# Performance work log

Hardware: AMD Instinct MI355X
Metric: run time of the kernel (lower is better)

Reference implementation:

```python
import jax, jax.numpy as jnp
import numpy as np

B, SQ, SK, D = 8, 2048, 768, 768  # SK must equal D for layer_combine concat to typecheck


def setup_inputs() -> dict:
    key = jax.random.key(0)
    ks = jax.random.split(key, 13)
    s = 0.02
    return {
        "query": jax.random.normal(ks[0], (B, SQ, D), jnp.float32),
        "key_matrix": jax.random.normal(ks[1], (B, SK, D), jnp.float32),
        "value_matrix": jax.random.normal(ks[2], (B, SK, D), jnp.float32),
        "prev_layer": jax.random.normal(ks[3], (SK, D), jnp.float32) * s,
        "attention_mask": jax.random.randint(ks[4], (B, 1, SK), 0, 2, jnp.int32),
        "Wq": jax.random.normal(ks[5], (D, D), jnp.float32) * s,
        "bq": jax.random.normal(ks[6], (D,), jnp.float32) * s,
        "Wk": jax.random.normal(ks[7], (D, D), jnp.float32) * s,
        "bk": jax.random.normal(ks[8], (D,), jnp.float32) * s,
        "Wv": jax.random.normal(ks[9], (D, D), jnp.float32) * s,
        "bv": jax.random.normal(ks[10], (D,), jnp.float32) * s,
        "Wc": jax.random.normal(ks[11], (D, 2 * D), jnp.float32) * s,
        "bc": jax.random.normal(ks[12], (D,), jnp.float32) * s,
    }


def reference(query, key_matrix, value_matrix, prev_layer, attention_mask,
              Wq, bq, Wk, bk, Wv, bv, Wc, bc):
    # Linear projections (torch Linear: x @ W.T + b)
    Q = query @ Wq.T + bq                      # [B, SQ, D]
    K = key_matrix @ Wk.T + bk                 # [B, SK, D]
    V = value_matrix @ Wv.T + bv               # computed but unused when prev_layer given (faithful)
    scale = 1.0 / np.sqrt(D).astype(np.float32)
    scores = jnp.einsum('bqd,bkd->bqk', Q, K) * scale  # [B, SQ, SK]
    scores = jnp.where(attention_mask == 0, jnp.float32(-1e9), scores)
    # prev-layer integration: matmul + concat + linear combine
    layer_attn = scores @ prev_layer           # [B, SQ, D]
    combined = jnp.concatenate([scores, layer_attn], axis=-1)  # [B, SQ, 2D]
    out = combined @ Wc.T + bc                 # [B, SQ, D]
    return out
```

## Files before the change

kernel.cpp:

```cpp
#include <hip/hip_runtime.h>
#include <hip/hip_bf16.h>


typedef __attribute__((ext_vector_type(8))) short short8;
typedef __attribute__((ext_vector_type(4))) float f32x4;

#define SCALE 0.03608439182435161f

__device__ inline unsigned short f2bf(float x) {
  unsigned int u = __builtin_bit_cast(unsigned int, x);
  u = (u + 0x7fffu + ((u >> 16) & 1u)) >> 16;
  return (unsigned short)u;
}
__device__ inline float bf2f(unsigned short h) {
  return __builtin_bit_cast(float, ((unsigned int)h) << 16);
}

__global__ void k_cvt(const float* __restrict__ s, unsigned short* __restrict__ d, int n4) {
  int i = blockIdx.x * 256 + threadIdx.x;
  if (i >= n4) return;
  float4 v = reinterpret_cast<const float4*>(s)[i];
  reinterpret_cast<ushort4*>(d)[i] = make_ushort4(f2bf(v.x), f2bf(v.y), f2bf(v.z), f2bf(v.w));
}

__global__ void k_prep(const float* __restrict__ Wk, const float* __restrict__ prev,
                       const float* __restrict__ Wc,
                       unsigned short* __restrict__ Wk_bf,
                       unsigned short* __restrict__ prev_bf,
                       unsigned short* __restrict__ Wc2_bf) {
  int g = blockIdx.x;
  int region = g / 576;
  int idx = (g - region * 576) * 256 + threadIdx.x;
  float4 v;
  unsigned short* dst;
  if (region == 0)      { v = reinterpret_cast<const float4*>(Wk)[idx];   dst = Wk_bf; }
  else if (region == 1) { v = reinterpret_cast<const float4*>(prev)[idx]; dst = prev_bf; }
  else {
    int r = idx / 192, c4 = (idx - r * 192) * 4;
    v = *reinterpret_cast<const float4*>(Wc + (long long)r * 1536 + 768 + c4);
    dst = Wc2_bf;
  }
  reinterpret_cast<ushort4*>(dst)[idx] = make_ushort4(f2bf(v.x), f2bf(v.y), f2bf(v.z), f2bf(v.w));
}

__global__ void k_transpose(const float* __restrict__ src, unsigned short* __restrict__ dst) {
  __shared__ float t[64][65];
  int bx = blockIdx.x * 64, by = blockIdx.y * 64;
  int tx = threadIdx.x & 63, ty = threadIdx.x >> 6;
  #pragma unroll
  for (int i = 0; i < 64; i += 4)
    t[ty + i][tx] = src[(long long)(by + ty + i) * 768 + bx + tx];
  __syncthreads();
  #pragma unroll
  for (int i = 0; i < 64; i += 4)
    dst[(long long)(bx + ty + i) * 768 + by + tx] = f2bf(t[tx][ty + i]);
}

template <int MODE, int BM, int BN>
__global__ __launch_bounds__(256) void gemm_nt(
    const unsigned short* __restrict__ A, long long aStr, int lda,
    const unsigned short* __restrict__ B, long long bStr, int ldb,
    float* __restrict__ Cf, unsigned short* __restrict__ Cbf,
    long long cStr, int ldc,
    const float* __restrict__ aux, const int* __restrict__ mask)
{
  constexpr int BK = 64;
  constexpr int MI = BM / 32;
  constexpr int NJ = BN / 32;
  constexpr int AG = BM * 8, BG = BN * 8;
  __shared__ __align__(16) char As[BM * BK * 2];
  __shared__ __align__(16) char Bs[BN * BK * 2];

  const int gx = gridDim.x, gy = gridDim.y;
  const int nwg = gx * gy * (int)gridDim.z;
  int lin = blockIdx.x + gx * (blockIdx.y + gy * blockIdx.z);
  int qq = nwg >> 3, rr = nwg & 7, xcd = lin & 7, loc = lin >> 3;
  int swz = (xcd < rr ? xcd * (qq + 1) : rr * (qq + 1) + (xcd - rr) * qq) + loc;
  int bz = swz / (gx * gy);
  int rem = swz - bz * gx * gy;
  int by = rem / gx, bx = rem - by * gx;

  const int b = bz;
  const unsigned short* Ab = A + (long long)b * aStr;
  const unsigned short* Bb = B + (long long)b * bStr;
  const int m0 = by * BM, n0 = bx * BN;

  const int tid = threadIdx.x;
  const int w = tid >> 6, lane = tid & 63;
  const int wr = w >> 1, wc = w & 1;
  const int fr = lane & 15, fq = lane >> 4;

  f32x4 acc[MI][NJ] = {};

  for (int kt = 0; kt < 768; kt += BK) {
    __syncthreads();
    #pragma unroll
    for (int t = 0; t < AG / 256; ++t) {
      int g = t * 256 + tid;
      int row = g >> 3, s = g & 7;
      int sg = (s - row) & 7;
      const unsigned short* ga = Ab + (long long)(m0 + row) * lda + kt + sg * 8;
      __builtin_amdgcn_global_load_lds(
          (const __attribute__((address_space(1))) void*)ga,
          (__attribute__((address_space(3))) void*)(As + g * 16), 16, 0, 0);
    }
    #pragma unroll
    for (int t = 0; t < BG / 256; ++t) {
      int g = t * 256 + tid;
      int row = g >> 3, s = g & 7;
      int sg = (s - row) & 7;
      const unsigned short* gb = Bb + (long long)(n0 + row) * ldb + kt + sg * 8;
      __builtin_amdgcn_global_load_lds(
          (const __attribute__((address_space(1))) void*)gb,
          (__attribute__((address_space(3))) void*)(Bs + g * 16), 16, 0, 0);
    }
    __syncthreads();

    #pragma unroll
    for (int kk = 0; kk < 2; ++kk) {
      short8 af[MI], bfr[NJ];
      #pragma unroll
      for (int i = 0; i < MI; ++i) {
        int r = wr * (BM / 2) + i * 16 + fr;
        int sgi = ((kk * 4 + fq) + r) & 7;
        af[i] = *reinterpret_cast<const short8*>(As + r * 128 + sgi * 16);
      }
      #pragma unroll
      for (int j = 0; j < NJ; ++j) {
        int r = wc * (BN / 2) + j * 16 + fr;
        int sgj = ((kk * 4 + fq) + r) & 7;
        bfr[j] = *reinterpret_cast<const short8*>(Bs + r * 128 + sgj * 16);
      }
      #pragma unroll
      for (int i = 0; i < MI; ++i)
        #pragma unroll
        for (int j = 0; j < NJ; ++j)
          acc[i][j] = __builtin_amdgcn_mfma_f32_16x16x32_bf16(af[i], bfr[j], acc[i][j], 0, 0, 0);
    }
  }

  const int* mb = (MODE == 1) ? (mask + b * 768) : nullptr;
  #pragma unroll
  for (int i = 0; i < MI; ++i)
    #pragma unroll
    for (int j = 0; j < NJ; ++j)
      #pragma unroll
      for (int r = 0; r < 4; ++r) {
        int row = m0 + wr * (BM / 2) + i * 16 + fq * 4 + r;
        int col = n0 + wc * (BN / 2) + j * 16 + fr;
        float v = acc[i][j][r];
        if constexpr (MODE == 0) {
          v += aux[(long long)row * 1536 + col];
          Cf[(long long)row * 768 + col] = v;
          Cbf[(long long)row * 768 + col] = f2bf(v);
        } else if constexpr (MODE == 1) {
          v += aux[row];
          if (mb[col] == 0) v = 0.0f;
          Cbf[(long long)b * cStr + (long long)row * ldc + col] = f2bf(v);
        } else if constexpr (MODE == 2 || MODE == 3) {
          Cbf[(long long)b * cStr + (long long)row * ldc + col] = f2bf(v);
        } else {
          Cf[(long long)b * cStr + (long long)row * ldc + col] = v * SCALE + aux[b * 768 + col];
        }
      }
}

__global__ void k_row(const float* __restrict__ Mt, const unsigned short* __restrict__ Nt,
                      const int* __restrict__ mask, const float* __restrict__ bq,
                      const float* __restrict__ bc, float* __restrict__ row)
{
  int gw = blockIdx.x * 4 + (threadIdx.x >> 6);
  int lane = threadIdx.x & 63;
  int b = gw / 768;
  int d2 = gw - b * 768;
  if (b >= 8) return;
  const int* mb = mask + b * 768;
  const float* mrow = Mt + (long long)d2 * 768;
  const unsigned short* nrow = Nt + ((long long)b * 768 + d2) * 768;
  float sm = 0.f, sb = 0.f;
  for (int k = lane; k < 768; k += 64) {
    if (mb[k] == 0) sm += mrow[k];
    sb += bq[k] * bf2f(nrow[k]);
  }
  #pragma unroll
  for (int off = 32; off > 0; off >>= 1) {
    sm += __shfl_down(sm, off, 64);
    sb += __shfl_down(sb, off, 64);
  }
  if (lane == 0) row[gw] = bc[d2] - 1e9f * sm + SCALE * sb;
}

extern "C" void kernel_launch(void* const* d_in, const int* in_sizes, int n_in,
                              void* d_out, int out_size, void* d_ws, size_t ws_size,
                              hipStream_t stream)
{
  const float* query = (const float*)d_in[0];
  const float* key   = (const float*)d_in[1];
  const float* prev  = (const float*)d_in[3];
  const int*   mask  = (const int*)d_in[4];
  const float* Wq    = (const float*)d_in[5];
  const float* bq    = (const float*)d_in[6];
  const float* Wk    = (const float*)d_in[7];
  const float* bk    = (const float*)d_in[8];
  const float* Wc    = (const float*)d_in[11];
  const float* bc    = (const float*)d_in[12];
  float* out = (float*)d_out;

  char* p = (char*)d_ws;
  size_t off = 0;
  auto alloc = [&](size_t bytes) {
    char* r = p + off;
    off += (bytes + 255) & ~(size_t)255;
    return r;
  };
  unsigned short* query_bf = (unsigned short*)alloc(12582912ull * 2);
  unsigned short* key_bf   = (unsigned short*)alloc(4718592ull * 2);
  unsigned short* prev_bf  = (unsigned short*)alloc(589824ull * 2);
  unsigned short* Wk_bf    = (unsigned short*)alloc(589824ull * 2);
  unsigned short* Wc2_bf   = (unsigned short*)alloc(589824ull * 2);
  unsigned short* WqT_bf   = (unsigned short*)alloc(589824ull * 2);
  float*          Mt_f     = (float*)alloc(589824ull * 4);
  unsigned short* Mt_bf    = (unsigned short*)alloc(589824ull * 2);
  unsigned short* KzT_bf   = (unsigned short*)alloc(4718592ull * 2);
  unsigned short* Nt_bf    = (unsigned short*)alloc(4718592ull * 2);
  float*          rowv     = (float*)alloc(6144ull * 4);
  unsigned short* Pt_bf    = KzT_bf;
  (void)ws_size; (void)in_sizes; (void)n_in; (void)out_size;

  k_cvt<<<dim3(12288), dim3(256), 0, stream>>>(query, query_bf, 3145728);
  k_cvt<<<dim3(4608),  dim3(256), 0, stream>>>(key, key_bf, 1179648);
  k_prep<<<dim3(1728), dim3(256), 0, stream>>>(Wk, prev, Wc, Wk_bf, prev_bf, Wc2_bf);
  k_transpose<<<dim3(12, 12), dim3(256), 0, stream>>>(Wq, WqT_bf);

  gemm_nt<0, 64, 64><<<dim3(12, 12, 1), dim3(256), 0, stream>>>(
      Wc2_bf, 0ll, 768, prev_bf, 0ll, 768, Mt_f, Mt_bf, 0ll, 768, Wc, (const int*)nullptr);
  gemm_nt<1, 64, 64><<<dim3(12, 12, 8), dim3(256), 0, stream>>>(
      Wk_bf, 0ll, 768, key_bf, 589824ll, 768, (float*)nullptr, KzT_bf, 589824ll, 768, bk, mask);
  gemm_nt<2, 64, 64><<<dim3(12, 12, 8), dim3(256), 0, stream>>>(
      Mt_bf, 0ll, 768, KzT_bf, 589824ll, 768, (float*)nullptr, Nt_bf, 589824ll, 768,
      (const float*)nullptr, (const int*)nullptr);
  k_row<<<dim3(1536), dim3(256), 0, stream>>>(Mt_f, Nt_bf, mask, bq, bc, rowv);
  gemm_nt<3, 64, 64><<<dim3(12, 12, 8), dim3(256), 0, stream>>>(
      Nt_bf, 589824ll, 768, WqT_bf, 0ll, 768, (float*)nullptr, Pt_bf, 589824ll, 768,
      (const float*)nullptr, (const int*)nullptr);
  gemm_nt<4, 128, 128><<<dim3(6, 16, 8), dim3(256), 0, stream>>>(
      query_bf, 1572864ll, 768, Pt_bf, 589824ll, 768, out, (unsigned short*)nullptr,
      1572864ll, 768, rowv, (const int*)nullptr);
}
```

Before: 127.1 us.

## Double-buffer LDS tiles in GEMM to overlap global loads with MFMA compute

Splits the GEMM main loop into stage and compute lambdas and doubles the LDS buffers, so the next K tile is issued via global_load_lds while MFMAs run on the current tile. This removes one barrier per iteration and is meant to hide global memory latency. Doubling LDS usage per block may lower occupancy. Correctness relies on the single barrier also covering completion of the async LDS loads.

```diff
diff --git a/kernel.cpp b/kernel.cpp
--- a/kernel.cpp
+++ b/kernel.cpp
@@ -67,9 +67,11 @@
   constexpr int BK = 64;
   constexpr int MI = BM / 32;
   constexpr int NJ = BN / 32;
-  constexpr int AG = BM * 8, BG = BN * 8;
-  __shared__ __align__(16) char As[BM * BK * 2];
-  __shared__ __align__(16) char Bs[BN * BK * 2];
+  constexpr int AGT = BM * 8 / 256;
+  constexpr int BGT = BN * 8 / 256;
+  constexpr int ASZ = BM * BK * 2, BSZ = BN * BK * 2;
+  __shared__ __align__(16) char As[2 * ASZ];
+  __shared__ __align__(16) char Bs[2 * BSZ];
 
   const int gx = gridDim.x, gy = gridDim.y;
   const int nwg = gx * gy * (int)gridDim.z;
@@ -92,30 +94,34 @@
 
   f32x4 acc[MI][NJ] = {};
 
-  for (int kt = 0; kt < 768; kt += BK) {
-    __syncthreads();
-    #pragma unroll
-    for (int t = 0; t < AG / 256; ++t) {
+  auto stage = [&](int buf, int kt) {
+    char* ad = As + buf * ASZ;
+    char* bd = Bs + buf * BSZ;
+    #pragma unroll
+    for (int t = 0; t < AGT; ++t) {
       int g = t * 256 + tid;
       int row = g >> 3, s = g & 7;
       int sg = (s - row) & 7;
       const unsigned short* ga = Ab + (long long)(m0 + row) * lda + kt + sg * 8;
       __builtin_amdgcn_global_load_lds(
           (const __attribute__((address_space(1))) void*)ga,
-          (__attribute__((address_space(3))) void*)(As + g * 16), 16, 0, 0);
+          (__attribute__((address_space(3))) void*)(ad + g * 16), 16, 0, 0);
     }
     #pragma unroll
-    for (int t = 0; t < BG / 256; ++t) {
+    for (int t = 0; t < BGT; ++t) {
       int g = t * 256 + tid;
       int row = g >> 3, s = g & 7;
       int sg = (s - row) & 7;
       const unsigned short* gb = Bb + (long long)(n0 + row) * ldb + kt + sg * 8;
       __builtin_amdgcn_global_load_lds(
           (const __attribute__((address_space(1))) void*)gb,
-          (__attribute__((address_space(3))) void*)(Bs + g * 16), 16, 0, 0);
+          (__attribute__((address_space(3))) void*)(bd + g * 16), 16, 0, 0);
     }
-    __syncthreads();
-
+  };
+
+  auto compute = [&](int buf) {
+    const char* as = As + buf * ASZ;
+    const char* bs = Bs + buf * BSZ;
     #pragma unroll
     for (int kk = 0; kk < 2; ++kk) {
       short8 af[MI], bfr[NJ];
@@ -123,13 +129,13 @@
       for (int i = 0; i < MI; ++i) {
         int r = wr * (BM / 2) + i * 16 + fr;
         int sgi = ((kk * 4 + fq) + r) & 7;
-        af[i] = *reinterpret_cast<const short8*>(As + r * 128 + sgi * 16);
+        af[i] = *reinterpret_cast<const short8*>(as + r * 128 + sgi * 16);
       }
       #pragma unroll
       for (int j = 0; j < NJ; ++j) {
         int r = wc * (BN / 2) + j * 16 + fr;
         int sgj = ((kk * 4 + fq) + r) & 7;
-        bfr[j] = *reinterpret_cast<const short8*>(Bs + r * 128 + sgj * 16);
+        bfr[j] = *reinterpret_cast<const short8*>(bs + r * 128 + sgj * 16);
       }
       #pragma unroll
       for (int i = 0; i < MI; ++i)
@@ -137,7 +143,18 @@
         for (int j = 0; j < NJ; ++j)
           acc[i][j] = __builtin_amdgcn_mfma_f32_16x16x32_bf16(af[i], bfr[j], acc[i][j], 0, 0, 0);
     }
-  }
+  };
+
+  stage(0, 0);
+  __syncthreads();
+  int cur = 0;
+  for (int kt = BK; kt < 768; kt += BK) {
+    stage(cur ^ 1, kt);
+    compute(cur);
+    __syncthreads();
+    cur ^= 1;
+  }
+  compute(cur);
 
   const int* mb = (MODE == 1) ? (mask + b * 768) : nullptr;
   #pragma unroll
```

Result: slower. 142.5 us (+12.1%).

## Reassociate projection chain and read fp32 query directly in final GEMM

Applied to the files above, without the earlier changes.

The weight product Wq^T·Wk is precomputed once, masked keys are transposed and zeroed in one pass, and the bias cross-terms are folded into rank-1 epilogues and small reduction kernels. The final GEMM now loads fp32 query straight into LDS and truncates it to bf16 in registers. This removes the separate query and key conversion passes and the per-batch Wk projection. In exchange it doubles LDS traffic for the A operand, adds several small launches, and uses truncation instead of round-to-nearest for query.

```diff
diff --git a/kernel.cpp b/kernel.cpp
--- a/kernel.cpp
+++ b/kernel.cpp
@@ -4,6 +4,7 @@
 
 typedef __attribute__((ext_vector_type(8))) short short8;
 typedef __attribute__((ext_vector_type(4))) float f32x4;
+typedef __attribute__((ext_vector_type(4))) unsigned int u32x4;
 
 #define SCALE 0.03608439182435161f
 
@@ -15,17 +16,12 @@
 __device__ inline float bf2f(unsigned short h) {
   return __builtin_bit_cast(float, ((unsigned int)h) << 16);
 }
-
-__global__ void k_cvt(const float* __restrict__ s, unsigned short* __restrict__ d, int n4) {
-  int i = blockIdx.x * 256 + threadIdx.x;
-  if (i >= n4) return;
-  float4 v = reinterpret_cast<const float4*>(s)[i];
-  reinterpret_cast<ushort4*>(d)[i] = make_ushort4(f2bf(v.x), f2bf(v.y), f2bf(v.z), f2bf(v.w));
-}
-
-__global__ void k_prep(const float* __restrict__ Wk, const float* __restrict__ prev,
-                       const float* __restrict__ Wc,
-                       unsigned short* __restrict__ Wk_bf,
+__device__ inline unsigned int pack_trunc(float hi, float lo) {
+  return __builtin_amdgcn_perm(__builtin_bit_cast(unsigned int, hi),
+                               __builtin_bit_cast(unsigned int, lo), 0x07060302u);
+}
+
+__global__ void k_prep(const float* __restrict__ prev, const float* __restrict__ Wc,
                        unsigned short* __restrict__ prev_bf,
                        unsigned short* __restrict__ Wc2_bf) {
   int g = blockIdx.x;
@@ -33,8 +29,7 @@
   int idx = (g - region * 576) * 256 + threadIdx.x;
   float4 v;
   unsigned short* dst;
-  if (region == 0)      { v = reinterpret_cast<const float4*>(Wk)[idx];   dst = Wk_bf; }
-  else if (region == 1) { v = reinterpret_cast<const float4*>(prev)[idx]; dst = prev_bf; }
+  if (region == 0) { v = reinterpret_cast<const float4*>(prev)[idx]; dst = prev_bf; }
   else {
     int r = idx / 192, c4 = (idx - r * 192) * 4;
     v = *reinterpret_cast<const float4*>(Wc + (long long)r * 1536 + 768 + c4);
@@ -43,8 +38,11 @@
   reinterpret_cast<ushort4*>(dst)[idx] = make_ushort4(f2bf(v.x), f2bf(v.y), f2bf(v.z), f2bf(v.w));
 }
 
-__global__ void k_transpose(const float* __restrict__ src, unsigned short* __restrict__ dst) {
+__global__ void k_tposeW(const float* __restrict__ Wq, const float* __restrict__ Wk,
+                         unsigned short* __restrict__ WqT, unsigned short* __restrict__ WkT) {
   __shared__ float t[64][65];
+  const float* src = blockIdx.z ? Wk : Wq;
+  unsigned short* dst = blockIdx.z ? WkT : WqT;
   int bx = blockIdx.x * 64, by = blockIdx.y * 64;
   int tx = threadIdx.x & 63, ty = threadIdx.x >> 6;
   #pragma unroll
@@ -56,19 +54,102 @@
     dst[(long long)(bx + ty + i) * 768 + by + tx] = f2bf(t[tx][ty + i]);
 }
 
-template <int MODE, int BM, int BN>
+__global__ void k_cvtz(const float* __restrict__ key, const int* __restrict__ mask,
+                       unsigned short* __restrict__ keyzT) {
+  __shared__ float t[64][65];
+  int b = blockIdx.z;
+  const float* src = key + (long long)b * 589824;
+  unsigned short* dst = keyzT + (long long)b * 589824;
+  const int* mb = mask + b * 768;
+  int bx = blockIdx.x * 64, by = blockIdx.y * 64;
+  int tx = threadIdx.x & 63, ty = threadIdx.x >> 6;
+  #pragma unroll
+  for (int i = 0; i < 64; i += 4) {
+    float v = src[(long long)(by + ty + i) * 768 + bx + tx];
+    t[ty + i][tx] = mb[by + ty + i] ? v : 0.0f;
+  }
+  __syncthreads();
+  #pragma unroll
+  for (int i = 0; i < 64; i += 4)
+    dst[(long long)(bx + ty + i) * 768 + by + tx] = f2bf(t[tx][ty + i]);
+}
+
+__global__ void k_scalars(const unsigned short* __restrict__ WqT,
+                          const unsigned short* __restrict__ WkT,
+                          const float* __restrict__ bk, const float* __restrict__ bq,
+                          float* __restrict__ u, float* __restrict__ w3) {
+  int gw = blockIdx.x * 4 + (threadIdx.x >> 6);
+  int lane = threadIdx.x & 63;
+  if (gw >= 1536) return;
+  const unsigned short* wrow = (gw < 768) ? (WqT + (long long)gw * 768)
+                                          : (WkT + (long long)(gw - 768) * 768);
+  const float* vec = (gw < 768) ? bk : bq;
+  float s = 0.f;
+  for (int j = lane; j < 768; j += 64) s += bf2f(wrow[j]) * vec[j];
+  #pragma unroll
+  for (int off = 32; off > 0; off >>= 1) s += __shfl_down(s, off, 64);
+  if (lane == 0) { if (gw < 768) u[gw] = s; else w3[gw - 768] = s; }
+}
+
+__global__ void k_scol(const float* __restrict__ Mt, const int* __restrict__ mask,
+                       float* __restrict__ s1, float* __restrict__ sm0) {
+  int gw = blockIdx.x * 4 + (threadIdx.x >> 6);
+  int lane = threadIdx.x & 63;
+  int b = gw / 768, d2 = gw - b * 768;
+  if (b >= 8) return;
+  const int* mb = mask + b * 768;
+  const float* mrow = Mt + (long long)d2 * 768;
+  float a1 = 0.f, a0 = 0.f;
+  for (int k = lane; k < 768; k += 64) {
+    float v = mrow[k];
+    if (mb[k]) a1 += v; else a0 += v;
+  }
+  #pragma unroll
+  for (int off = 32; off > 0; off >>= 1) {
+    a1 += __shfl_down(a1, off, 64);
+    a0 += __shfl_down(a0, off, 64);
+  }
+  if (lane == 0) { s1[gw] = a1; sm0[gw] = a0; }
+}
+
+__global__ void k_row(const unsigned short* __restrict__ Tt, const float* __restrict__ w3,
+                      const float* __restrict__ s1, const float* __restrict__ sm0,
+                      const float* __restrict__ bq, const float* __restrict__ bk,
+                      const float* __restrict__ bc, float* __restrict__ row) {
+  int gw = blockIdx.x * 4 + (threadIdx.x >> 6);
+  int lane = threadIdx.x & 63;
+  int b = gw / 768, d2 = gw - b * 768;
+  if (b >= 8) return;
+  const unsigned short* trow = Tt + ((long long)b * 768 + d2) * 768;
+  float st = 0.f, sbb = 0.f;
+  for (int j = lane; j < 768; j += 64) {
+    st += bf2f(trow[j]) * w3[j];
+    sbb += bq[j] * bk[j];
+  }
+  #pragma unroll
+  for (int off = 32; off > 0; off >>= 1) {
+    st += __shfl_down(st, off, 64);
+    sbb += __shfl_down(sbb, off, 64);
+  }
+  if (lane == 0)
+    row[gw] = bc[d2] - 1e9f * sm0[gw] + SCALE * (st + sbb * s1[gw]);
+}
+
+template <int MODE, int BM, int BN, int AF32>
 __global__ __launch_bounds__(256) void gemm_nt(
-    const unsigned short* __restrict__ A, long long aStr, int lda,
+    const void* __restrict__ A, long long aStr, int lda,
     const unsigned short* __restrict__ B, long long bStr, int ldb,
     float* __restrict__ Cf, unsigned short* __restrict__ Cbf,
     long long cStr, int ldc,
-    const float* __restrict__ aux, const int* __restrict__ mask)
+    const float* __restrict__ aux, const float* __restrict__ aux2)
 {
   constexpr int BK = 64;
-  constexpr int MI = BM / 32;
-  constexpr int NJ = BN / 32;
-  constexpr int AG = BM * 8, BG = BN * 8;
-  __shared__ __align__(16) char As[BM * BK * 2];
+  constexpr int EA = AF32 ? 4 : 2;
+  constexpr int AGR = BK * EA / 16;
+  constexpr int MI = BM / 32, NJ = BN / 32;
+  constexpr int AGT = BM * AGR / 256, BGT = BN * 8 / 256;
+  constexpr int ARB = BK * EA;
+  __shared__ __align__(16) char As[BM * BK * EA];
   __shared__ __align__(16) char Bs[BN * BK * 2];
 
   const int gx = gridDim.x, gy = gridDim.y;
@@ -81,7 +162,7 @@
   int by = rem / gx, bx = rem - by * gx;
 
   const int b = bz;
-  const unsigned short* Ab = A + (long long)b * aStr;
+  const char* Ab = (const char*)A + (long long)b * aStr * EA;
   const unsigned short* Bb = B + (long long)b * bStr;
   const int m0 = by * BM, n0 = bx * BN;
 
@@ -95,17 +176,17 @@
   for (int kt = 0; kt < 768; kt += BK) {
     __syncthreads();
     #pragma unroll
-    for (int t = 0; t < AG / 256; ++t) {
+    for (int t = 0; t < AGT; ++t) {
       int g = t * 256 + tid;
-      int row = g >> 3, s = g & 7;
-      int sg = (s - row) & 7;
-      const unsigned short* ga = Ab + (long long)(m0 + row) * lda + kt + sg * 8;
+      int row = g / AGR, s = g & (AGR - 1);
+      int sg = (s - row) & (AGR - 1);
+      long long boff = ((long long)(m0 + row) * lda + kt) * EA + sg * 16;
       __builtin_amdgcn_global_load_lds(
-          (const __attribute__((address_space(1))) void*)ga,
+          (const __attribute__((address_space(1))) void*)(Ab + boff),
           (__attribute__((address_space(3))) void*)(As + g * 16), 16, 0, 0);
     }
     #pragma unroll
-    for (int t = 0; t < BG / 256; ++t) {
+    for (int t = 0; t < BGT; ++t) {
       int g = t * 256 + tid;
       int row = g >> 3, s = g & 7;
       int sg = (s - row) & 7;
@@ -122,8 +203,19 @@
       #pragma unroll
       for (int i = 0; i < MI; ++i) {
         int r = wr * (BM / 2) + i * 16 + fr;
-        int sgi = ((kk * 4 + fq) + r) & 7;
-        af[i] = *reinterpret_cast<const short8*>(As + r * 128 + sgi * 16);
+        if constexpr (AF32) {
+          const f32x4* base = (const f32x4*)(As + r * ARB);
+          int gidx = kk * 8 + fq * 2;
+          f32x4 x = base[(gidx + r) & 15];
+          f32x4 y = base[(gidx + 1 + r) & 15];
+          unsigned int p0 = pack_trunc(x[1], x[0]), p1 = pack_trunc(x[3], x[2]);
+          unsigned int p2 = pack_trunc(y[1], y[0]), p3 = pack_trunc(y[3], y[2]);
+          u32x4 u4 = {p0, p1, p2, p3};
+          af[i] = __builtin_bit_cast(short8, u4);
+        } else {
+          int sgi = ((kk * 4 + fq) + r) & 7;
+          af[i] = *reinterpret_cast<const short8*>(As + r * 128 + sgi * 16);
+        }
       }
       #pragma unroll
       for (int j = 0; j < NJ; ++j) {
@@ -139,7 +231,6 @@
     }
   }
 
-  const int* mb = (MODE == 1) ? (mask + b * 768) : nullptr;
   #pragma unroll
   for (int i = 0; i < MI; ++i)
     #pragma unroll
@@ -153,41 +244,15 @@
           v += aux[(long long)row * 1536 + col];
           Cf[(long long)row * 768 + col] = v;
           Cbf[(long long)row * 768 + col] = f2bf(v);
-        } else if constexpr (MODE == 1) {
-          v += aux[row];
-          if (mb[col] == 0) v = 0.0f;
+        } else if constexpr (MODE == 2) {
           Cbf[(long long)b * cStr + (long long)row * ldc + col] = f2bf(v);
-        } else if constexpr (MODE == 2 || MODE == 3) {
+        } else if constexpr (MODE == 5) {
+          v += aux[b * 768 + row] * aux2[col];
           Cbf[(long long)b * cStr + (long long)row * ldc + col] = f2bf(v);
         } else {
           Cf[(long long)b * cStr + (long long)row * ldc + col] = v * SCALE + aux[b * 768 + col];
         }
       }
-}
-
-__global__ void k_row(const float* __restrict__ Mt, const unsigned short* __restrict__ Nt,
-                      const int* __restrict__ mask, const float* __restrict__ bq,
-                      const float* __restrict__ bc, float* __restrict__ row)
-{
-  int gw = blockIdx.x * 4 + (threadIdx.x >> 6);
-  int lane = threadIdx.x & 63;
-  int b = gw / 768;
-  int d2 = gw - b * 768;
-  if (b >= 8) return;
-  const int* mb = mask + b * 768;
-  const float* mrow = Mt + (long long)d2 * 768;
-  const unsigned short* nrow = Nt + ((long long)b * 768 + d2) * 768;
-  float sm = 0.f, sb = 0.f;
-  for (int k = lane; k < 768; k += 64) {
-    if (mb[k] == 0) sm += mrow[k];
-    sb += bq[k] * bf2f(nrow[k]);
-  }
-  #pragma unroll
-  for (int off = 32; off > 0; off >>= 1) {
-    sm += __shfl_down(sm, off, 64);
-    sb += __shfl_down(sb, off, 64);
-  }
-  if (lane == 0) row[gw] = bc[d2] - 1e9f * sm + SCALE * sb;
 }
 
 extern "C" void kernel_launch(void* const* d_in, const int* in_sizes, int n_in,
@@ -213,37 +278,43 @@
     off += (bytes + 255) & ~(size_t)255;
     return r;
   };
-  unsigned short* query_bf = (unsigned short*)alloc(12582912ull * 2);
-  unsigned short* key_bf   = (unsigned short*)alloc(4718592ull * 2);
+  unsigned short* keyzT_bf = (unsigned short*)alloc(4718592ull * 2);
+  unsigned short* WqT_bf   = (unsigned short*)alloc(589824ull * 2);
+  unsigned short* WkT_bf   = (unsigned short*)alloc(589824ull * 2);
   unsigned short* prev_bf  = (unsigned short*)alloc(589824ull * 2);
-  unsigned short* Wk_bf    = (unsigned short*)alloc(589824ull * 2);
   unsigned short* Wc2_bf   = (unsigned short*)alloc(589824ull * 2);
-  unsigned short* WqT_bf   = (unsigned short*)alloc(589824ull * 2);
   float*          Mt_f     = (float*)alloc(589824ull * 4);
   unsigned short* Mt_bf    = (unsigned short*)alloc(589824ull * 2);
-  unsigned short* KzT_bf   = (unsigned short*)alloc(4718592ull * 2);
-  unsigned short* Nt_bf    = (unsigned short*)alloc(4718592ull * 2);
+  unsigned short* W2_bf    = (unsigned short*)alloc(589824ull * 2);
+  unsigned short* Tt_bf    = (unsigned short*)alloc(4718592ull * 2);
+  unsigned short* Pt_bf    = (unsigned short*)alloc(4718592ull * 2);
+  float*          s1f      = (float*)alloc(6144ull * 4);
+  float*          sm0f     = (float*)alloc(6144ull * 4);
+  float*          uv       = (float*)alloc(768ull * 4);
+  float*          w3v      = (float*)alloc(768ull * 4);
   float*          rowv     = (float*)alloc(6144ull * 4);
-  unsigned short* Pt_bf    = KzT_bf;
   (void)ws_size; (void)in_sizes; (void)n_in; (void)out_size;
 
-  k_cvt<<<dim3(12288), dim3(256), 0, stream>>>(query, query_bf, 3145728);
-  k_cvt<<<dim3(4608),  dim3(256), 0, stream>>>(key, key_bf, 1179648);
-  k_prep<<<dim3(1728), dim3(256), 0, stream>>>(Wk, prev, Wc, Wk_bf, prev_bf, Wc2_bf);
-  k_transpose<<<dim3(12, 12), dim3(256), 0, stream>>>(Wq, WqT_bf);
-
-  gemm_nt<0, 64, 64><<<dim3(12, 12, 1), dim3(256), 0, stream>>>(
-      Wc2_bf, 0ll, 768, prev_bf, 0ll, 768, Mt_f, Mt_bf, 0ll, 768, Wc, (const int*)nullptr);
-  gemm_nt<1, 64, 64><<<dim3(12, 12, 8), dim3(256), 0, stream>>>(
-      Wk_bf, 0ll, 768, key_bf, 589824ll, 768, (float*)nullptr, KzT_bf, 589824ll, 768, bk, mask);
-  gemm_nt<2, 64, 64><<<dim3(12, 12, 8), dim3(256), 0, stream>>>(
-      Mt_bf, 0ll, 768, KzT_bf, 589824ll, 768, (float*)nullptr, Nt_bf, 589824ll, 768,
-      (const float*)nullptr, (const int*)nullptr);
-  k_row<<<dim3(1536), dim3(256), 0, stream>>>(Mt_f, Nt_bf, mask, bq, bc, rowv);
-  gemm_nt<3, 64, 64><<<dim3(12, 12, 8), dim3(256), 0, stream>>>(
-      Nt_bf, 589824ll, 768, WqT_bf, 0ll, 768, (float*)nullptr, Pt_bf, 589824ll, 768,
-      (const float*)nullptr, (const int*)nullptr);
-  gemm_nt<4, 128, 128><<<dim3(6, 16, 8), dim3(256), 0, stream>>>(
-      query_bf, 1572864ll, 768, Pt_bf, 589824ll, 768, out, (unsigned short*)nullptr,
-      1572864ll, 768, rowv, (const int*)nullptr);
-}
+  k_tposeW<<<dim3(12, 12, 2), dim3(256), 0, stream>>>(Wq, Wk, WqT_bf, WkT_bf);
+  k_prep<<<dim3(1152), dim3(256), 0, stream>>>(prev, Wc, prev_bf, Wc2_bf);
+  k_cvtz<<<dim3(12, 12, 8), dim3(256), 0, stream>>>(key, mask, keyzT_bf);
+
+  gemm_nt<0, 64, 64, 0><<<dim3(12, 12, 1), dim3(256), 0, stream>>>(
+      (const void*)Wc2_bf, 0ll, 768, prev_bf, 0ll, 768, Mt_f, Mt_bf, 0ll, 768,
+      Wc, (const float*)nullptr);
+  gemm_nt<2, 64, 64, 0><<<dim3(12, 12, 1), dim3(256), 0, stream>>>(
+      (const void*)WqT_bf, 0ll, 768, WkT_bf, 0ll, 768, (float*)nullptr, W2_bf, 0ll, 768,
+      (const float*)nullptr, (const float*)nullptr);
+  k_scalars<<<dim3(384), dim3(256), 0, stream>>>(WqT_bf, WkT_bf, bk, bq, uv, w3v);
+  k_scol<<<dim3(1536), dim3(256), 0, stream>>>(Mt_f, mask, s1f, sm0f);
+  gemm_nt<2, 64, 64, 0><<<dim3(12, 12, 8), dim3(256), 0, stream>>>(
+      (const void*)Mt_bf, 0ll, 768, keyzT_bf, 589824ll, 768, (float*)nullptr, Tt_bf,
+      589824ll, 768, (const float*)nullptr, (const float*)nullptr);
+  gemm_nt<5, 64, 64, 0><<<dim3(12, 12, 8), dim3(256), 0, stream>>>(
+      (const void*)Tt_bf, 589824ll, 768, W2_bf, 0ll, 768, (float*)nullptr, Pt_bf,
+      589824ll, 768, s1f, uv);
+  k_row<<<dim3(1536), dim3(256), 0, stream>>>(Tt_bf, w3v, s1f, sm0f, bq, bk, bc, rowv);
+  gemm_nt<4, 128, 128, 1><<<dim3(6, 16, 8), dim3(256), 0, stream>>>(
+      (const void*)query, 1572864ll, 768, Pt_bf, 589824ll, 768, out,
+      (unsigned short*)nullptr, 1572864ll, 768, rowv, (const float*)nullptr);
+}
```

Measured after the change: 123.4 us. 1.03x faster.
